# Kernel tuning notes

Measured on AMD Instinct MI355X. Metric: run time of the kernel, lower is better.

Reference implementation:

```python
import jax, jax.numpy as jnp
import numpy as np

DEPTH = 4  # truncation depth of the signature


def setup_inputs() -> dict:
    key = jax.random.key(0)
    # (N, L, C) batch of paths
    path = jax.random.normal(key, (64, 512, 8), dtype=jnp.float32)
    return {"path": path}


def _signature(path, depth):
    """Truncated path signature: exp(dx_1) (x) exp(dx_2) (x) ... via Chen's relation.

    Signature state is kept as a tuple of flattened tensor levels, level k has
    shape (N, C**k). Combining a signature S with exp(z) gives, at level k:
        sum_{j=0}^{k} S_{k-j} (x) z^{(x)j} / j!   (with S_0 = 1)
    """
    N, L, C = path.shape
    # increments, scanned over the stream dim: (L-1, N, C)
    diffs = jnp.swapaxes(path[:, 1:] - path[:, :-1], 0, 1)

    def step(sig, z):
        # powers[j-1] = z^{(x)j} / j!, flattened to (N, C**j)
        powers = [z]
        for j in range(2, depth + 1):
            powers.append((powers[-1][:, :, None] * z[:, None, :]).reshape(N, -1) / j)
        new = []
        for k in range(1, depth + 1):
            term = sig[k - 1] + powers[k - 1]  # j=0 and j=k terms
            for j in range(1, k):
                # S_{k-j} (x) z^{(x)j}/j!
                term = term + (sig[k - j - 1][:, :, None]
                               * powers[j - 1][:, None, :]).reshape(N, C ** k)
            new.append(term)
        return tuple(new), None

    # identity element of the tensor algebra: all levels >= 1 are zero
    init = tuple(jnp.zeros((N, C ** k), dtype=path.dtype) for k in range(1, depth + 1))
    sig, _ = jax.lax.scan(step, init, diffs)
    # (N, C + C^2 + ... + C^depth)
    return jnp.concatenate(sig, axis=-1)


def reference(path) -> jnp.ndarray:
    return _signature(path, DEPTH)
```

## Files before the change

kernel.cpp:

```cpp
#include <hip/hip_runtime.h>


typedef float f2 __attribute__((ext_vector_type(2)));

#define NB 64
#define LP 512
#define SIG 4680
#define O2 8
#define O3 72
#define O4 584
#define SB 648
#define L123_F4 146

#define A3IDX(pq, r) (72 + (pq) * 9 + (r))
#define B3IDX(x, y, z) (72 + (x) * 72 + (y) * 8 + (z))

__device__ __forceinline__ f2 mkf2(float x, float y) { f2 r; r[0] = x; r[1] = y; return r; }

__device__ __forceinline__ void prod_core(
    f2 (&a4)[8], const f2 (&b4)[8],
    const float* Ap, float* Aq, const float* B,
    int tid, int w, int l, int a, int b)
{
    const int c0 = 2 * w;
    const float A1   = Ap[a];
    const float A2   = Ap[O2 + a * 8 + b];
    const float A3_0 = Ap[A3IDX(a * 8 + b, c0)];
    const float A3_1 = Ap[A3IDX(a * 8 + b, c0 + 1)];
    f2 b1p[4], b2p[8], b3p[8];
    *(float4*)&b1p[0] = *(const float4*)(B);
    *(float4*)&b1p[2] = *(const float4*)(B + 4);
    #pragma unroll
    for (int i = 0; i < 4; ++i) {
        *(float4*)&b2p[2 * i] = *(const float4*)(B + O2 + c0 * 8 + 4 * i);
        *(float4*)&b3p[2 * i] = *(const float4*)(B + B3IDX(b, c0, 0) + 4 * i);
    }
    #pragma unroll
    for (int cc = 0; cc < 2; ++cc) {
        const float A3c = cc ? A3_1 : A3_0;
        #pragma unroll
        for (int j = 0; j < 4; ++j)
            a4[cc * 4 + j] += b4[cc * 4 + j] + A3c * b1p[j]
                            + A2 * b2p[cc * 4 + j] + A1 * b3p[cc * 4 + j];
    }
    const int f0 = 2 * tid;
    const int pp = f0 >> 6, qq = (f0 >> 3) & 7, rr = f0 & 7;
    const float A1p  = Ap[pp];
    const float A2pq = Ap[O2 + pp * 8 + qq];
    Aq[A3IDX(pp * 8 + qq, rr)]     = Ap[A3IDX(pp * 8 + qq, rr)]
        + B[B3IDX(pp, qq, rr)]     + A2pq * B[rr]     + A1p * B[O2 + qq * 8 + rr];
    Aq[A3IDX(pp * 8 + qq, rr + 1)] = Ap[A3IDX(pp * 8 + qq, rr + 1)]
        + B[B3IDX(pp, qq, rr + 1)] + A2pq * B[rr + 1] + A1p * B[O2 + qq * 8 + rr + 1];
    if (tid < 64) Aq[O2 + tid] = Ap[O2 + tid] + B[O2 + tid] + Ap[tid >> 3] * B[tid & 7];
    if (tid < 8)  Aq[tid] = Ap[tid] + B[tid];
}

__global__ __launch_bounds__(256) void k1_sig(const float* __restrict__ path,
                                              float* __restrict__ ws)
{
    __shared__ __align__(16) float zbuf[128 * 8];
    __shared__ __align__(16) float sA[2][SB];
    __shared__ __align__(16) float sLb[3][SB];
    __shared__ __align__(16) float4 sT[4][1024];

    const int tid = threadIdx.x;
    const int n = blockIdx.x >> 2;
    const int g = blockIdx.x & 3;

    {
        const int r = tid >> 1, h = tid & 1;
        const int t = g * 128 + r;
        const float4* p4 = (const float4*)path + (size_t)n * (LP * 2);
        float4 z4 = make_float4(0.f, 0.f, 0.f, 0.f);
        if (t < LP - 1) {
            float4 x0 = p4[t * 2 + h];
            float4 x1 = p4[t * 2 + 2 + h];
            z4 = make_float4(x1.x - x0.x, x1.y - x0.y, x1.z - x0.z, x1.w - x0.w);
        }
        ((float4*)zbuf)[tid] = z4;
    }
    __syncthreads();

    const int w = tid >> 6, l = tid & 63;
    const int a = l >> 3, b = l & 7;
    const int f0 = 2 * tid;

    float s1 = 0.f, s2 = 0.f;
    f2 s3p[4], s4p[32];
    #pragma unroll
    for (int i = 0; i < 4; ++i) s3p[i] = mkf2(0.f, 0.f);
    #pragma unroll
    for (int e = 0; e < 32; ++e) s4p[e] = mkf2(0.f, 0.f);

    const float* zw = zbuf + w * (32 * 8);
    #pragma unroll 4
    for (int s = 0; s < 32; ++s) {
        const float* zs = zw + s * 8;
        f2 zp[4];
        #pragma unroll
        for (int j = 0; j < 4; ++j) zp[j] = ((const f2*)zs)[j];
        const float za  = zs[a];
        const float zbv = zs[b];
        const float B4 = zbv * (za * (1.f/24.f) + s1 * (1.f/6.f)) + s2 * 0.5f;
        const float G3 = zbv * (za * (1.f/6.f)  + s1 * 0.5f)      + s2;
        f2 Acp[4];
        #pragma unroll
        for (int i = 0; i < 4; ++i) Acp[i] = B4 * zp[i] + s3p[i];
        #pragma unroll
        for (int c = 0; c < 8; ++c) {
            const float Ac = Acp[c >> 1][c & 1];
            #pragma unroll
            for (int j = 0; j < 4; ++j) s4p[c * 4 + j] += Ac * zp[j];
        }
        #pragma unroll
        for (int i = 0; i < 4; ++i) s3p[i] += G3 * zp[i];
        s2 += zbv * (za * 0.5f + s1);
        s1 += za;
    }

    if (w == 0) {
        if (b == 0) sA[0][a] = s1;
        sA[0][O2 + l] = s2;
        #pragma unroll
        for (int c = 0; c < 8; ++c) sA[0][A3IDX(l, c)] = s3p[c >> 1][c & 1];
    } else {
        float* SL = sLb[w - 1];
        if (b == 0) SL[a] = s1;
        SL[O2 + l] = s2;
        *(float4*)&SL[B3IDX(a, b, 0)] = make_float4(s3p[0][0], s3p[0][1], s3p[1][0], s3p[1][1]);
        *(float4*)&SL[B3IDX(a, b, 4)] = make_float4(s3p[2][0], s3p[2][1], s3p[3][0], s3p[3][1]);
    }
    #pragma unroll
    for (int i = 0; i < 16; ++i)
        sT[w][i * 64 + l] = make_float4(s4p[2*i][0], s4p[2*i][1], s4p[2*i+1][0], s4p[2*i+1][1]);
    __syncthreads();

    f2 a4[8], b4[8];
    #pragma unroll
    for (int k = 0; k < 4; ++k) {
        float4 v = sT[0][(w * 4 + k) * 64 + l];
        a4[2*k] = mkf2(v.x, v.y); a4[2*k+1] = mkf2(v.z, v.w);
        float4 u = sT[1][(w * 4 + k) * 64 + l];
        b4[2*k] = mkf2(u.x, u.y); b4[2*k+1] = mkf2(u.z, u.w);
    }
    prod_core(a4, b4, sA[0], sA[1], sLb[0], tid, w, l, a, b);
    __syncthreads();
    #pragma unroll
    for (int k = 0; k < 4; ++k) {
        float4 u = sT[2][(w * 4 + k) * 64 + l];
        b4[2*k] = mkf2(u.x, u.y); b4[2*k+1] = mkf2(u.z, u.w);
    }
    prod_core(a4, b4, sA[1], sA[0], sLb[1], tid, w, l, a, b);
    __syncthreads();
    #pragma unroll
    for (int k = 0; k < 4; ++k) {
        float4 u = sT[3][(w * 4 + k) * 64 + l];
        b4[2*k] = mkf2(u.x, u.y); b4[2*k+1] = mkf2(u.z, u.w);
    }
    prod_core(a4, b4, sA[0], sA[1], sLb[2], tid, w, l, a, b);
    __syncthreads();

    float* dst = ws + (size_t)blockIdx.x * SIG;
    if (tid < O3) dst[tid] = sA[1][tid];
    dst[O3 + f0]     = sA[1][A3IDX(f0 >> 3, f0 & 7)];
    dst[O3 + f0 + 1] = sA[1][A3IDX(f0 >> 3, (f0 & 7) + 1)];
    float4* dT = (float4*)(dst + O4);
    #pragma unroll
    for (int k = 0; k < 4; ++k)
        dT[(w * 4 + k) * 64 + l] = make_float4(a4[2*k][0], a4[2*k][1], a4[2*k+1][0], a4[2*k+1][1]);
}

__global__ __launch_bounds__(256) void k2_final(const float* __restrict__ ws,
                                                float* __restrict__ out)
{
    __shared__ __align__(16) float sA[2][SB];
    __shared__ __align__(16) float sLb[3][SB];

    const int tid = threadIdx.x;
    const int n = blockIdx.x;
    const int w = tid >> 6, l = tid & 63;
    const int a = l >> 3, b = l & 7;
    const int f0 = 2 * tid;
    const float* base = ws + (size_t)n * 4 * SIG;

    if (tid < O3) sA[0][tid] = base[tid];
    sA[0][A3IDX(f0 >> 3, f0 & 7)]       = base[O3 + f0];
    sA[0][A3IDX(f0 >> 3, (f0 & 7) + 1)] = base[O3 + f0 + 1];
    #pragma unroll
    for (int m = 1; m <= 3; ++m) {
        if (tid < L123_F4) {
            float4 v = ((const float4*)(base + (size_t)m * SIG))[tid];
            int d4;
            if (tid < 18) d4 = tid;
            else { const int j = tid - 18; d4 = 18 + (j >> 4) * 18 + (j & 15); }
            ((float4*)sLb[m - 1])[d4] = v;
        }
    }
    f2 a4[8], b4A[8], b4B[8], b4C[8];
    #pragma unroll
    for (int k = 0; k < 4; ++k) {
        const int ti = (w * 4 + k) * 64 + l;
        float4 v = ((const float4*)(base + O4))[ti];
        a4[2*k] = mkf2(v.x, v.y); a4[2*k+1] = mkf2(v.z, v.w);
        float4 u1 = ((const float4*)(base + SIG + O4))[ti];
        b4A[2*k] = mkf2(u1.x, u1.y); b4A[2*k+1] = mkf2(u1.z, u1.w);
        float4 u2 = ((const float4*)(base + 2 * SIG + O4))[ti];
        b4B[2*k] = mkf2(u2.x, u2.y); b4B[2*k+1] = mkf2(u2.z, u2.w);
        float4 u3 = ((const float4*)(base + 3 * SIG + O4))[ti];
        b4C[2*k] = mkf2(u3.x, u3.y); b4C[2*k+1] = mkf2(u3.z, u3.w);
    }
    __syncthreads();

    prod_core(a4, b4A, sA[0], sA[1], sLb[0], tid, w, l, a, b);
    __syncthreads();
    prod_core(a4, b4B, sA[1], sA[0], sLb[1], tid, w, l, a, b);
    __syncthreads();
    prod_core(a4, b4C, sA[0], sA[1], sLb[2], tid, w, l, a, b);
    __syncthreads();

    float* dst = out + (size_t)n * SIG;
    if (tid < O3) dst[tid] = sA[1][tid];
    dst[O3 + f0]     = sA[1][A3IDX(f0 >> 3, f0 & 7)];
    dst[O3 + f0 + 1] = sA[1][A3IDX(f0 >> 3, (f0 & 7) + 1)];
    float4* d4p = (float4*)(dst + O4);
    #pragma unroll
    for (int k = 0; k < 4; ++k)
        d4p[l * 16 + w * 4 + k] = make_float4(a4[2*k][0], a4[2*k][1], a4[2*k+1][0], a4[2*k+1][1]);
}

extern "C" void kernel_launch(void* const* d_in, const int* in_sizes, int n_in,
                              void* d_out, int out_size, void* d_ws, size_t ws_size,
                              hipStream_t stream) {
    const float* path = (const float*)d_in[0];
    float* out = (float*)d_out;
    float* ws  = (float*)d_ws;

    k1_sig<<<NB * 4, 256, 0, stream>>>(path, ws);
    k2_final<<<NB, 256, 0, stream>>>(ws, out);
}
```

Measured before the change: 18.77 us.

## Split final combine kernel across four blocks per batch element

The second kernel now launches four blocks per path instead of one. Each block handles a quarter of the level-4 tensor with 8 outputs per thread instead of 32. Every block redundantly recomputes levels 1-3 in shared memory, and only block 0 writes them. This raises parallelism from 64 blocks to 256 on a GPU with many CUs, at the cost of duplicated low-level loads and compute, and launches the level-4 global loads before the shared-memory fills.

```diff
diff --git a/kernel.cpp b/kernel.cpp
--- a/kernel.cpp
+++ b/kernel.cpp
@@ -43,6 +43,33 @@
             a4[cc * 4 + j] += b4[cc * 4 + j] + A3c * b1p[j]
                             + A2 * b2p[cc * 4 + j] + A1 * b3p[cc * 4 + j];
     }
+    const int f0 = 2 * tid;
+    const int pp = f0 >> 6, qq = (f0 >> 3) & 7, rr = f0 & 7;
+    const float A1p  = Ap[pp];
+    const float A2pq = Ap[O2 + pp * 8 + qq];
+    Aq[A3IDX(pp * 8 + qq, rr)]     = Ap[A3IDX(pp * 8 + qq, rr)]
+        + B[B3IDX(pp, qq, rr)]     + A2pq * B[rr]     + A1p * B[O2 + qq * 8 + rr];
+    Aq[A3IDX(pp * 8 + qq, rr + 1)] = Ap[A3IDX(pp * 8 + qq, rr + 1)]
+        + B[B3IDX(pp, qq, rr + 1)] + A2pq * B[rr + 1] + A1p * B[O2 + qq * 8 + rr + 1];
+    if (tid < 64) Aq[O2 + tid] = Ap[O2 + tid] + B[O2 + tid] + Ap[tid >> 3] * B[tid & 7];
+    if (tid < 8)  Aq[tid] = Ap[tid] + B[tid];
+}
+
+__device__ __forceinline__ void prod_core_q(
+    f2 (&a4)[2], const f2 (&b4)[2],
+    const float* Ap, float* Aq, const float* B,
+    int tid, int a, int b, int c, int dh)
+{
+    const float A1  = Ap[a];
+    const float A2  = Ap[O2 + a * 8 + b];
+    const float A3c = Ap[A3IDX(a * 8 + b, c)];
+    f2 b1p[2], b2p[2], b3p[2];
+    *(float4*)&b1p[0] = *(const float4*)(B + dh);
+    *(float4*)&b2p[0] = *(const float4*)(B + O2 + c * 8 + dh);
+    *(float4*)&b3p[0] = *(const float4*)(B + B3IDX(b, c, dh));
+    #pragma unroll
+    for (int j = 0; j < 2; ++j)
+        a4[j] += b4[j] + A3c * b1p[j] + A2 * b2p[j] + A1 * b3p[j];
     const int f0 = 2 * tid;
     const int pp = f0 >> 6, qq = (f0 >> 3) & 7, rr = f0 & 7;
     const float A1p  = Ap[pp];
@@ -177,11 +204,27 @@
     __shared__ __align__(16) float sLb[3][SB];
 
     const int tid = threadIdx.x;
-    const int n = blockIdx.x;
-    const int w = tid >> 6, l = tid & 63;
-    const int a = l >> 3, b = l & 7;
+    const int n  = blockIdx.x >> 2;
+    const int w4 = blockIdx.x & 3;
+    const int a = tid >> 5, b = (tid >> 2) & 7, q = tid & 3;
+    const int cc = q >> 1, dh4 = q & 1;
+    const int c  = 2 * w4 + cc;
+    const int dh = dh4 * 4;
     const int f0 = 2 * tid;
     const float* base = ws + (size_t)n * 4 * SIG;
+
+    const int ti = (w4 * 4 + cc * 2 + dh4) * 64 + (a * 8 + b);
+    f2 a4[2], b4A[2], b4B[2], b4C[2];
+    {
+        float4 v  = ((const float4*)(base + O4))[ti];
+        a4[0] = mkf2(v.x, v.y);  a4[1] = mkf2(v.z, v.w);
+        float4 u1 = ((const float4*)(base + SIG + O4))[ti];
+        b4A[0] = mkf2(u1.x, u1.y); b4A[1] = mkf2(u1.z, u1.w);
+        float4 u2 = ((const float4*)(base + 2 * SIG + O4))[ti];
+        b4B[0] = mkf2(u2.x, u2.y); b4B[1] = mkf2(u2.z, u2.w);
+        float4 u3 = ((const float4*)(base + 3 * SIG + O4))[ti];
+        b4C[0] = mkf2(u3.x, u3.y); b4C[1] = mkf2(u3.z, u3.w);
+    }
 
     if (tid < O3) sA[0][tid] = base[tid];
     sA[0][A3IDX(f0 >> 3, f0 & 7)]       = base[O3 + f0];
@@ -196,36 +239,24 @@
             ((float4*)sLb[m - 1])[d4] = v;
         }
     }
-    f2 a4[8], b4A[8], b4B[8], b4C[8];
-    #pragma unroll
-    for (int k = 0; k < 4; ++k) {
-        const int ti = (w * 4 + k) * 64 + l;
-        float4 v = ((const float4*)(base + O4))[ti];
-        a4[2*k] = mkf2(v.x, v.y); a4[2*k+1] = mkf2(v.z, v.w);
-        float4 u1 = ((const float4*)(base + SIG + O4))[ti];
-        b4A[2*k] = mkf2(u1.x, u1.y); b4A[2*k+1] = mkf2(u1.z, u1.w);
-        float4 u2 = ((const float4*)(base + 2 * SIG + O4))[ti];
-        b4B[2*k] = mkf2(u2.x, u2.y); b4B[2*k+1] = mkf2(u2.z, u2.w);
-        float4 u3 = ((const float4*)(base + 3 * SIG + O4))[ti];
-        b4C[2*k] = mkf2(u3.x, u3.y); b4C[2*k+1] = mkf2(u3.z, u3.w);
-    }
-    __syncthreads();
-
-    prod_core(a4, b4A, sA[0], sA[1], sLb[0], tid, w, l, a, b);
-    __syncthreads();
-    prod_core(a4, b4B, sA[1], sA[0], sLb[1], tid, w, l, a, b);
-    __syncthreads();
-    prod_core(a4, b4C, sA[0], sA[1], sLb[2], tid, w, l, a, b);
+    __syncthreads();
+
+    prod_core_q(a4, b4A, sA[0], sA[1], sLb[0], tid, a, b, c, dh);
+    __syncthreads();
+    prod_core_q(a4, b4B, sA[1], sA[0], sLb[1], tid, a, b, c, dh);
+    __syncthreads();
+    prod_core_q(a4, b4C, sA[0], sA[1], sLb[2], tid, a, b, c, dh);
     __syncthreads();
 
     float* dst = out + (size_t)n * SIG;
-    if (tid < O3) dst[tid] = sA[1][tid];
-    dst[O3 + f0]     = sA[1][A3IDX(f0 >> 3, f0 & 7)];
-    dst[O3 + f0 + 1] = sA[1][A3IDX(f0 >> 3, (f0 & 7) + 1)];
+    if (w4 == 0) {
+        if (tid < O3) dst[tid] = sA[1][tid];
+        dst[O3 + f0]     = sA[1][A3IDX(f0 >> 3, f0 & 7)];
+        dst[O3 + f0 + 1] = sA[1][A3IDX(f0 >> 3, (f0 & 7) + 1)];
+    }
     float4* d4p = (float4*)(dst + O4);
-    #pragma unroll
-    for (int k = 0; k < 4; ++k)
-        d4p[l * 16 + w * 4 + k] = make_float4(a4[2*k][0], a4[2*k][1], a4[2*k+1][0], a4[2*k+1][1]);
+    d4p[((a * 8 + b) * 8 + c) * 2 + dh4] =
+        make_float4(a4[0][0], a4[0][1], a4[1][0], a4[1][1]);
 }
 
 extern "C" void kernel_launch(void* const* d_in, const int* in_sizes, int n_in,
@@ -236,5 +267,5 @@
     float* ws  = (float*)d_ws;
 
     k1_sig<<<NB * 4, 256, 0, stream>>>(path, ws);
-    k2_final<<<NB, 256, 0, stream>>>(ws, out);
-}
+    k2_final<<<NB * 4, 256, 0, stream>>>(ws, out);
+}
```

After: 18.34 us. 2.3% less time.

## Defer all Chen combines to second kernel, split level-4 across four blocks

Applied to the files above, without the earlier changes.

The first kernel now writes each wave's 32-step partial signature straight to workspace, dropping the in-block shared-memory Chen combine and its barriers. The second kernel takes all 16 partials per path and runs 4 blocks per path instead of 1. Each block rebuilds the prefix levels 1-3 chain redundantly in shared memory, then folds all 15 level-4 combines for its quarter of the level-4 entries. This trades redundant low-level work and more workspace traffic for shorter serial chains and more parallelism in the second kernel.

```diff
diff --git a/kernel.cpp b/kernel.cpp
--- a/kernel.cpp
+++ b/kernel.cpp
@@ -8,61 +8,18 @@
 #define SIG 4680
 #define O2 8
 #define O3 72
-#define O4 584
+#define WSS 4744
+#define WL4 162
 #define SB 648
-#define L123_F4 146
 
-#define A3IDX(pq, r) (72 + (pq) * 9 + (r))
 #define B3IDX(x, y, z) (72 + (x) * 72 + (y) * 8 + (z))
 
 __device__ __forceinline__ f2 mkf2(float x, float y) { f2 r; r[0] = x; r[1] = y; return r; }
-
-__device__ __forceinline__ void prod_core(
-    f2 (&a4)[8], const f2 (&b4)[8],
-    const float* Ap, float* Aq, const float* B,
-    int tid, int w, int l, int a, int b)
-{
-    const int c0 = 2 * w;
-    const float A1   = Ap[a];
-    const float A2   = Ap[O2 + a * 8 + b];
-    const float A3_0 = Ap[A3IDX(a * 8 + b, c0)];
-    const float A3_1 = Ap[A3IDX(a * 8 + b, c0 + 1)];
-    f2 b1p[4], b2p[8], b3p[8];
-    *(float4*)&b1p[0] = *(const float4*)(B);
-    *(float4*)&b1p[2] = *(const float4*)(B + 4);
-    #pragma unroll
-    for (int i = 0; i < 4; ++i) {
-        *(float4*)&b2p[2 * i] = *(const float4*)(B + O2 + c0 * 8 + 4 * i);
-        *(float4*)&b3p[2 * i] = *(const float4*)(B + B3IDX(b, c0, 0) + 4 * i);
-    }
-    #pragma unroll
-    for (int cc = 0; cc < 2; ++cc) {
-        const float A3c = cc ? A3_1 : A3_0;
-        #pragma unroll
-        for (int j = 0; j < 4; ++j)
-            a4[cc * 4 + j] += b4[cc * 4 + j] + A3c * b1p[j]
-                            + A2 * b2p[cc * 4 + j] + A1 * b3p[cc * 4 + j];
-    }
-    const int f0 = 2 * tid;
-    const int pp = f0 >> 6, qq = (f0 >> 3) & 7, rr = f0 & 7;
-    const float A1p  = Ap[pp];
-    const float A2pq = Ap[O2 + pp * 8 + qq];
-    Aq[A3IDX(pp * 8 + qq, rr)]     = Ap[A3IDX(pp * 8 + qq, rr)]
-        + B[B3IDX(pp, qq, rr)]     + A2pq * B[rr]     + A1p * B[O2 + qq * 8 + rr];
-    Aq[A3IDX(pp * 8 + qq, rr + 1)] = Ap[A3IDX(pp * 8 + qq, rr + 1)]
-        + B[B3IDX(pp, qq, rr + 1)] + A2pq * B[rr + 1] + A1p * B[O2 + qq * 8 + rr + 1];
-    if (tid < 64) Aq[O2 + tid] = Ap[O2 + tid] + B[O2 + tid] + Ap[tid >> 3] * B[tid & 7];
-    if (tid < 8)  Aq[tid] = Ap[tid] + B[tid];
-}
 
 __global__ __launch_bounds__(256) void k1_sig(const float* __restrict__ path,
                                               float* __restrict__ ws)
 {
     __shared__ __align__(16) float zbuf[128 * 8];
-    __shared__ __align__(16) float sA[2][SB];
-    __shared__ __align__(16) float sLb[3][SB];
-    __shared__ __align__(16) float4 sT[4][1024];
-
     const int tid = threadIdx.x;
     const int n = blockIdx.x >> 2;
     const int g = blockIdx.x & 3;
@@ -83,7 +40,6 @@
 
     const int w = tid >> 6, l = tid & 63;
     const int a = l >> 3, b = l & 7;
-    const int f0 = 2 * tid;
 
     float s1 = 0.f, s2 = 0.f;
     f2 s3p[4], s4p[32];
@@ -118,114 +74,90 @@
         s1 += za;
     }
 
-    if (w == 0) {
-        if (b == 0) sA[0][a] = s1;
-        sA[0][O2 + l] = s2;
-        #pragma unroll
-        for (int c = 0; c < 8; ++c) sA[0][A3IDX(l, c)] = s3p[c >> 1][c & 1];
-    } else {
-        float* SL = sLb[w - 1];
-        if (b == 0) SL[a] = s1;
-        SL[O2 + l] = s2;
-        *(float4*)&SL[B3IDX(a, b, 0)] = make_float4(s3p[0][0], s3p[0][1], s3p[1][0], s3p[1][1]);
-        *(float4*)&SL[B3IDX(a, b, 4)] = make_float4(s3p[2][0], s3p[2][1], s3p[3][0], s3p[3][1]);
-    }
+    float* dst = ws + (size_t)(n * 16 + g * 4 + w) * WSS;
+    if (b == 0) dst[a] = s1;
+    dst[O2 + l] = s2;
+    *(float4*)&dst[B3IDX(a, b, 0)] = make_float4(s3p[0][0], s3p[0][1], s3p[1][0], s3p[1][1]);
+    *(float4*)&dst[B3IDX(a, b, 4)] = make_float4(s3p[2][0], s3p[2][1], s3p[3][0], s3p[3][1]);
+    float4* dT = (float4*)dst + WL4;
     #pragma unroll
     for (int i = 0; i < 16; ++i)
-        sT[w][i * 64 + l] = make_float4(s4p[2*i][0], s4p[2*i][1], s4p[2*i+1][0], s4p[2*i+1][1]);
-    __syncthreads();
-
-    f2 a4[8], b4[8];
-    #pragma unroll
-    for (int k = 0; k < 4; ++k) {
-        float4 v = sT[0][(w * 4 + k) * 64 + l];
-        a4[2*k] = mkf2(v.x, v.y); a4[2*k+1] = mkf2(v.z, v.w);
-        float4 u = sT[1][(w * 4 + k) * 64 + l];
-        b4[2*k] = mkf2(u.x, u.y); b4[2*k+1] = mkf2(u.z, u.w);
-    }
-    prod_core(a4, b4, sA[0], sA[1], sLb[0], tid, w, l, a, b);
-    __syncthreads();
-    #pragma unroll
-    for (int k = 0; k < 4; ++k) {
-        float4 u = sT[2][(w * 4 + k) * 64 + l];
-        b4[2*k] = mkf2(u.x, u.y); b4[2*k+1] = mkf2(u.z, u.w);
-    }
-    prod_core(a4, b4, sA[1], sA[0], sLb[1], tid, w, l, a, b);
-    __syncthreads();
-    #pragma unroll
-    for (int k = 0; k < 4; ++k) {
-        float4 u = sT[3][(w * 4 + k) * 64 + l];
-        b4[2*k] = mkf2(u.x, u.y); b4[2*k+1] = mkf2(u.z, u.w);
-    }
-    prod_core(a4, b4, sA[0], sA[1], sLb[2], tid, w, l, a, b);
-    __syncthreads();
-
-    float* dst = ws + (size_t)blockIdx.x * SIG;
-    if (tid < O3) dst[tid] = sA[1][tid];
-    dst[O3 + f0]     = sA[1][A3IDX(f0 >> 3, f0 & 7)];
-    dst[O3 + f0 + 1] = sA[1][A3IDX(f0 >> 3, (f0 & 7) + 1)];
-    float4* dT = (float4*)(dst + O4);
-    #pragma unroll
-    for (int k = 0; k < 4; ++k)
-        dT[(w * 4 + k) * 64 + l] = make_float4(a4[2*k][0], a4[2*k][1], a4[2*k+1][0], a4[2*k+1][1]);
+        dT[i * 64 + l] = make_float4(s4p[2*i][0], s4p[2*i][1], s4p[2*i+1][0], s4p[2*i+1][1]);
 }
 
 __global__ __launch_bounds__(256) void k2_final(const float* __restrict__ ws,
                                                 float* __restrict__ out)
 {
-    __shared__ __align__(16) float sA[2][SB];
-    __shared__ __align__(16) float sLb[3][SB];
+    __shared__ __align__(16) float sBuf[31][SB];
 
     const int tid = threadIdx.x;
-    const int n = blockIdx.x;
-    const int w = tid >> 6, l = tid & 63;
-    const int a = l >> 3, b = l & 7;
+    const int n  = blockIdx.x >> 2;
+    const int w4 = blockIdx.x & 3;
+    const int a = tid >> 5, b = (tid >> 2) & 7, q = tid & 3;
+    const int cc = q >> 1, dh4 = q & 1;
+    const int c  = 2 * w4 + cc;
+    const int dh = dh4 * 4;
     const int f0 = 2 * tid;
-    const float* base = ws + (size_t)n * 4 * SIG;
+    const int pp = f0 >> 6, qq = (f0 >> 3) & 7, rr = f0 & 7;
+    const float* base = ws + (size_t)n * 16 * WSS;
 
-    if (tid < O3) sA[0][tid] = base[tid];
-    sA[0][A3IDX(f0 >> 3, f0 & 7)]       = base[O3 + f0];
-    sA[0][A3IDX(f0 >> 3, (f0 & 7) + 1)] = base[O3 + f0 + 1];
+    const int ti = (w4 * 4 + cc * 2 + dh4) * 64 + (a * 8 + b);
+    f2 b4[16][2];
     #pragma unroll
-    for (int m = 1; m <= 3; ++m) {
-        if (tid < L123_F4) {
-            float4 v = ((const float4*)(base + (size_t)m * SIG))[tid];
-            int d4;
-            if (tid < 18) d4 = tid;
-            else { const int j = tid - 18; d4 = 18 + (j >> 4) * 18 + (j & 15); }
-            ((float4*)sLb[m - 1])[d4] = v;
-        }
+    for (int m = 0; m < 16; ++m) {
+        float4 u = ((const float4*)(base + (size_t)m * WSS))[WL4 + ti];
+        b4[m][0] = mkf2(u.x, u.y);
+        b4[m][1] = mkf2(u.z, u.w);
     }
-    f2 a4[8], b4A[8], b4B[8], b4C[8];
-    #pragma unroll
-    for (int k = 0; k < 4; ++k) {
-        const int ti = (w * 4 + k) * 64 + l;
-        float4 v = ((const float4*)(base + O4))[ti];
-        a4[2*k] = mkf2(v.x, v.y); a4[2*k+1] = mkf2(v.z, v.w);
-        float4 u1 = ((const float4*)(base + SIG + O4))[ti];
-        b4A[2*k] = mkf2(u1.x, u1.y); b4A[2*k+1] = mkf2(u1.z, u1.w);
-        float4 u2 = ((const float4*)(base + 2 * SIG + O4))[ti];
-        b4B[2*k] = mkf2(u2.x, u2.y); b4B[2*k+1] = mkf2(u2.z, u2.w);
-        float4 u3 = ((const float4*)(base + 3 * SIG + O4))[ti];
-        b4C[2*k] = mkf2(u3.x, u3.y); b4C[2*k+1] = mkf2(u3.z, u3.w);
+
+    for (int e = tid; e < 16 * 162; e += 256) {
+        const int m = e / 162, o = e - m * 162;
+        ((float4*)sBuf[m])[o] = ((const float4*)(base + (size_t)m * WSS))[o];
     }
     __syncthreads();
 
-    prod_core(a4, b4A, sA[0], sA[1], sLb[0], tid, w, l, a, b);
-    __syncthreads();
-    prod_core(a4, b4B, sA[1], sA[0], sLb[1], tid, w, l, a, b);
-    __syncthreads();
-    prod_core(a4, b4C, sA[0], sA[1], sLb[2], tid, w, l, a, b);
-    __syncthreads();
+    #pragma unroll 1
+    for (int j = 1; j <= 15; ++j) {
+        const float* A = (j == 1) ? sBuf[0] : sBuf[15 + j - 1];
+        const float* B = sBuf[j];
+        float* P = sBuf[15 + j];
+        const float A1p  = A[pp];
+        const float A2pq = A[O2 + pp * 8 + qq];
+        P[B3IDX(pp, qq, rr)]     = A[B3IDX(pp, qq, rr)]     + B[B3IDX(pp, qq, rr)]
+                                 + A2pq * B[rr]     + A1p * B[O2 + qq * 8 + rr];
+        P[B3IDX(pp, qq, rr + 1)] = A[B3IDX(pp, qq, rr + 1)] + B[B3IDX(pp, qq, rr + 1)]
+                                 + A2pq * B[rr + 1] + A1p * B[O2 + qq * 8 + rr + 1];
+        if (tid < 64) P[O2 + tid] = A[O2 + tid] + B[O2 + tid] + A[tid >> 3] * B[tid & 7];
+        if (tid < 8)  P[tid] = A[tid] + B[tid];
+        __syncthreads();
+    }
+
+    f2 a4[2] = { b4[0][0], b4[0][1] };
+    #pragma unroll
+    for (int j = 1; j <= 15; ++j) {
+        const float* Pm = (j == 1) ? sBuf[0] : sBuf[15 + j - 1];
+        const float* B  = sBuf[j];
+        const float A1  = Pm[a];
+        const float A2  = Pm[O2 + a * 8 + b];
+        const float A3c = Pm[B3IDX(a, b, c)];
+        f2 b1p[2], b2p[2], b3p[2];
+        *(float4*)&b1p[0] = *(const float4*)(B + dh);
+        *(float4*)&b2p[0] = *(const float4*)(B + O2 + c * 8 + dh);
+        *(float4*)&b3p[0] = *(const float4*)(B + B3IDX(b, c, dh));
+        #pragma unroll
+        for (int t2 = 0; t2 < 2; ++t2)
+            a4[t2] += b4[j][t2] + A3c * b1p[t2] + A2 * b2p[t2] + A1 * b3p[t2];
+    }
 
     float* dst = out + (size_t)n * SIG;
-    if (tid < O3) dst[tid] = sA[1][tid];
-    dst[O3 + f0]     = sA[1][A3IDX(f0 >> 3, f0 & 7)];
-    dst[O3 + f0 + 1] = sA[1][A3IDX(f0 >> 3, (f0 & 7) + 1)];
-    float4* d4p = (float4*)(dst + O4);
-    #pragma unroll
-    for (int k = 0; k < 4; ++k)
-        d4p[l * 16 + w * 4 + k] = make_float4(a4[2*k][0], a4[2*k][1], a4[2*k+1][0], a4[2*k+1][1]);
+    const float* PF = sBuf[30];
+    if (w4 == 0) {
+        if (tid < O3) dst[tid] = PF[tid];
+        dst[O3 + f0]     = PF[B3IDX(pp, qq, rr)];
+        dst[O3 + f0 + 1] = PF[B3IDX(pp, qq, rr + 1)];
+    }
+    ((float4*)(dst + 584))[((a * 8 + b) * 8 + c) * 2 + dh4] =
+        make_float4(a4[0][0], a4[0][1], a4[1][0], a4[1][1]);
 }
 
 extern "C" void kernel_launch(void* const* d_in, const int* in_sizes, int n_in,
@@ -236,5 +168,5 @@
     float* ws  = (float*)d_ws;
 
     k1_sig<<<NB * 4, 256, 0, stream>>>(path, ws);
-    k2_final<<<NB, 256, 0, stream>>>(ws, out);
+    k2_final<<<NB * 4, 256, 0, stream>>>(ws, out);
 }
```

New measurement: 30.54 us. 1.63x slower.
